# Kernel tuning notes

Measured on AMD Instinct MI355X. Metric: run time of the kernel, lower is better.

## Reference

```python
import jax, jax.numpy as jnp
import numpy as np

B = 8
FEAT = 256
HID = 256
NCLS = 80
SIZES = [(128, 128), (64, 64), (32, 32), (16, 16), (8, 8)]
DELTA_XY = 0.1   # dd_delta_range_xy
DELTA_WH = 2.0   # dd_delta_range_wh
PRIOR_P = 0.01   # prior_cls_prob


def _priors():
    # prior_cxcy: normalized grid centers per pyramid level (sine_pos_encodings id maps,
    # normalize=True with all-ones masks). prior_wh: (1/fW, 1/fH) per level.
    cxcy, wh = [], []
    for (h, w) in SIZES:
        cy = (jnp.arange(h, dtype=jnp.float32) + 0.5) / h
        cx = (jnp.arange(w, dtype=jnp.float32) + 0.5) / w
        gx, gy = jnp.meshgrid(cx, cy, indexing='xy')           # [h, w]
        cxcy.append(jnp.stack([gx, gy], axis=-1).reshape(h * w, 2))
        wh.append(jnp.broadcast_to(jnp.array([1.0 / w, 1.0 / h], jnp.float32), (h * w, 2)))
    return jnp.concatenate(cxcy, axis=0), jnp.concatenate(wh, axis=0)  # [N,2], [N,2]


def _mlp(x, Wh, bh, Wo, bo):
    # Linear(feat->hidden) + ReLU, then Linear(hidden->out)
    h = jax.nn.relu(jnp.einsum('bnf,hf->bnh', x, Wh) + bh)
    return jnp.einsum('bnh,oh->bno', h, Wo) + bo


def setup_inputs() -> dict:
    key = jax.random.key(0)
    ks = jax.random.split(key, 12)
    inp = {}
    for i, (h, w) in enumerate(SIZES):
        inp[f'fm{i}'] = jax.random.normal(ks[i], (B, FEAT, h, w), dtype=jnp.float32)
    s_in = 1.0 / np.sqrt(FEAT)
    s_h = 1.0 / np.sqrt(HID)
    bias_value = float(-np.log((1.0 - PRIOR_P) / PRIOR_P))
    inp['cls_Wh'] = jax.random.normal(ks[5], (HID, FEAT), dtype=jnp.float32) * s_in
    inp['cls_bh'] = jnp.zeros((HID,), jnp.float32)
    inp['cls_Wo'] = jax.random.normal(ks[6], (NCLS, HID), dtype=jnp.float32) * s_h
    inp['cls_bo'] = jnp.full((NCLS,), bias_value, jnp.float32)  # focal prior bias init
    inp['box_Wh'] = jax.random.normal(ks[7], (HID, FEAT), dtype=jnp.float32) * s_in
    inp['box_bh'] = jnp.zeros((HID,), jnp.float32)
    inp['box_Wo'] = jax.random.normal(ks[8], (4, HID), dtype=jnp.float32) * s_h
    inp['box_bo'] = jnp.zeros((4,), jnp.float32)  # zero-init box bias
    return inp


def reference(fm0, fm1, fm2, fm3, fm4,
              cls_Wh, cls_bh, cls_Wo, cls_bo,
              box_Wh, box_bh, box_Wo, box_bo):
    fms = [fm0, fm1, fm2, fm3, fm4]
    # obj_feats: concat of flatten(2).permute(0,2,1) -> [B, N, FEAT]
    obj_feats = jnp.concatenate(
        [f.reshape(B, FEAT, -1).transpose(0, 2, 1) for f in fms], axis=1)
    cls_logits = _mlp(obj_feats, cls_Wh, cls_bh, cls_Wo, cls_bo)   # [B, N, NCLS]
    box_logits = _mlp(obj_feats, box_Wh, box_bh, box_Wo, box_bo)   # [B, N, 4]
    box_deltas = jnp.tanh(box_logits)
    prior_cxcy, prior_wh = _priors()
    pred_cxcy = prior_cxcy[None] + DELTA_XY * box_deltas[:, :, :2]
    pred_wh = prior_wh[None] * (DELTA_WH ** box_deltas[:, :, 2:])
    # pack [cls_logits | pred_boxes(cxcywh)] -> [B, N, NCLS+4]
    return jnp.concatenate([cls_logits, pred_cxcy, pred_wh], axis=-1)
```

## Files before the change

### kernel.cpp

```cpp
#include <hip/hip_runtime.h>
#include <hip/hip_bf16.h>
#include <math.h>
#include <stdint.h>

#define NTOK 21824
#define NTILE128 171

typedef __attribute__((ext_vector_type(8)))  short bf16x8;
typedef __attribute__((ext_vector_type(4)))  float f32x4;
typedef __attribute__((ext_vector_type(16))) float f32x16;

__device__ __forceinline__ uint32_t f2bf(float f) {
    uint32_t u = __builtin_bit_cast(uint32_t, f);
    return (u + 0x7FFFu + ((u >> 16) & 1u)) >> 16;
}
__device__ __forceinline__ uint32_t pkbf2(float lo, float hi) {
    __hip_bfloat162 h = __float22bfloat162_rn(float2{lo, hi});
    uint32_t r; __builtin_memcpy(&r, &h, 4);
    return r;
}

#define WOFF_CWH 0
#define WOFF_BWH 65536
#define WOFF_CWO 131072
#define WOFF_BWO 151552

__global__ void prep_weights(const float* __restrict__ cWh, const float* __restrict__ cWo,
                             const float* __restrict__ bWh, const float* __restrict__ bWo,
                             uint16_t* __restrict__ ws) {
    int i = blockIdx.x * 256 + threadIdx.x;
    if (i >= 155648) return;
    uint32_t v;
    if (i < 65536)       v = f2bf(cWh[i]);
    else if (i < 131072) v = f2bf(bWh[i - 65536]);
    else if (i < 151552) v = f2bf(cWo[i - 131072]);
    else { int j = i - 151552; v = (j < 1024) ? f2bf(bWo[j]) : 0u; }
    ws[i] = (uint16_t)v;
}

__global__ __launch_bounds__(512, 4) void dfd_head(
    const float* __restrict__ fm0, const float* __restrict__ fm1,
    const float* __restrict__ fm2, const float* __restrict__ fm3,
    const float* __restrict__ fm4,
    const float* __restrict__ cls_bh, const float* __restrict__ cls_bo,
    const float* __restrict__ box_bh, const float* __restrict__ box_bo,
    const uint16_t* __restrict__ wbf,
    float* __restrict__ out)
{
    const int g    = blockIdx.x;
    const int s    = g & 15;
    const int tile = (g >> 4) * 8 + (s & 7);
    const int head = s >> 3;
    if (tile >= NTILE128) return;

    __shared__ uint16_t LB[128 * 256];
    uint16_t* Xs = LB;
    uint16_t* Hs = LB;

    const int tid  = threadIdx.x;
    const int lane = tid & 63;
    const int w    = tid >> 6;
    const int r    = lane & 15;
    const int q    = lane >> 4;
    const int col  = lane & 31;
    const int hi   = lane >> 5;
    const int n0   = tile * 128;
    const int b    = blockIdx.y;

    const float* fm; int off, ls;
    if      (n0 < 16384) { fm = fm0; off = 0;     ls = 7; }
    else if (n0 < 20480) { fm = fm1; off = 16384; ls = 6; }
    else if (n0 < 21504) { fm = fm2; off = 20480; ls = 5; }
    else if (n0 < 21760) { fm = fm3; off = 21504; ls = 4; }
    else                 { fm = fm4; off = 21760; ls = 3; }
    const int dim = 1 << ls;
    const int hw  = 1 << (2 * ls);
    const int p0  = n0 - off;
    const int T   = (n0 == 21760) ? 64 : 128;
    const int NT16 = T >> 4;

    {
        const int t  = tid & 127;
        const int fg = tid >> 7;
        const int sw = (t & 31) << 3;
        if (t < T) {
            const float* src = fm + (size_t)b * 256 * hw + p0 + t;
            #pragma unroll
            for (int i = 0; i < 8; ++i) {
                const int f0 = fg * 64 + i * 8;
                float x[8];
                #pragma unroll
                for (int e = 0; e < 8; ++e) x[e] = src[(size_t)(f0 + e) * hw];
                uint4 pk;
                pk.x = pkbf2(x[0], x[1]); pk.y = pkbf2(x[2], x[3]);
                pk.z = pkbf2(x[4], x[5]); pk.w = pkbf2(x[6], x[7]);
                *reinterpret_cast<uint4*>(&Xs[t * 256 + (f0 ^ sw)]) = pk;
            }
        }
    }
    __syncthreads();

    f32x16 acc[4];
    {
        #pragma unroll
        for (int nt = 0; nt < 4; ++nt)
            #pragma unroll
            for (int e = 0; e < 16; ++e) acc[nt][e] = 0.f;

        const int hhw = w * 32;
        const uint16_t* Wbase = wbf + (head ? WOFF_BWH : WOFF_CWH) + hhw * 256;
        const int kh = hi * 8;
        const uint16_t* Wr = Wbase + col * 256 + kh;
        const int sw0 = col << 3;

        #pragma unroll
        for (int ks = 0; ks < 16; ++ks) {
            const bf16x8 a = *(const bf16x8*)(Wr + ks * 16);
            const int kx = (ks * 16 + kh) ^ sw0;
            #pragma unroll
            for (int nt = 0; nt < 4; ++nt) {
                const bf16x8 x = *(const bf16x8*)&Xs[(nt * 32 + col) * 256 + kx];
                acc[nt] = __builtin_amdgcn_mfma_f32_32x32x16_bf16(a, x, acc[nt], 0, 0, 0);
            }
        }
    }
    __syncthreads();

    {
        const int hhw = w * 32;
        const float* bh_ = (head ? box_bh : cls_bh) + hhw;
        #pragma unroll
        for (int nt = 0; nt < 4; ++nt) {
            const int t   = nt * 32 + col;
            const int swt = (t & 15) << 4;
            #pragma unroll
            for (int g2 = 0; g2 < 4; ++g2) {
                const int hb = 8 * g2 + 4 * hi;
                const f32x4 bv = *(const f32x4*)(bh_ + hb);
                const float v0 = fmaxf(acc[nt][4 * g2 + 0] + bv[0], 0.f);
                const float v1 = fmaxf(acc[nt][4 * g2 + 1] + bv[1], 0.f);
                const float v2 = fmaxf(acc[nt][4 * g2 + 2] + bv[2], 0.f);
                const float v3 = fmaxf(acc[nt][4 * g2 + 3] + bv[3], 0.f);
                uint2 pk; pk.x = pkbf2(v0, v1); pk.y = pkbf2(v2, v3);
                *reinterpret_cast<uint2*>(&Hs[t * 256 + ((hhw + hb) ^ swt)]) = pk;
            }
        }
    }
    __syncthreads();

    if (head == 0) {
        if (w < 5) {
            const uint16_t* Bw = wbf + WOFF_CWO + (w * 16 + r) * 256 + q * 8;
            bf16x8 bfr[8];
            #pragma unroll
            for (int kq = 0; kq < 8; ++kq) bfr[kq] = *(const bf16x8*)(Bw + kq * 32);
            const float bo_l = cls_bo[w * 16 + r];
            #pragma unroll
            for (int tt = 0; tt < 8; ++tt) {
                if (tt < NT16) {
                    const int tr  = tt * 16 + r;
                    const int swt = (tr & 15) << 4;
                    const uint16_t* hrow = &Hs[tr * 256];
                    f32x4 c = {0.f, 0.f, 0.f, 0.f};
                    #pragma unroll
                    for (int kq = 0; kq < 8; ++kq) {
                        const bf16x8 a = *(const bf16x8*)&hrow[(kq * 32 + q * 8) ^ swt];
                        c = __builtin_amdgcn_mfma_f32_16x16x32_bf16(a, bfr[kq], c, 0, 0, 0);
                    }
                    #pragma unroll
                    for (int jj = 0; jj < 4; ++jj)
                        out[((size_t)b * NTOK + n0 + tt * 16 + q * 4 + jj) * 84 + w * 16 + r]
                            = c[jj] + bo_l;
                }
            }
        }
    } else {
        if (w < NT16) {
            const uint16_t* Bw = wbf + WOFF_BWO + r * 256 + q * 8;
            const int tr  = w * 16 + r;
            const int swt = (tr & 15) << 4;
            const uint16_t* hrow = &Hs[tr * 256];
            f32x4 c = {0.f, 0.f, 0.f, 0.f};
            #pragma unroll
            for (int kq = 0; kq < 8; ++kq) {
                const bf16x8 a   = *(const bf16x8*)&hrow[(kq * 32 + q * 8) ^ swt];
                const bf16x8 bfr = *(const bf16x8*)(Bw + kq * 32);
                c = __builtin_amdgcn_mfma_f32_16x16x32_bf16(a, bfr, c, 0, 0, 0);
            }
            if (r < 4) {
                const float bo_l = box_bo[r];
                const float inv  = 1.0f / (float)dim;
                #pragma unroll
                for (int jj = 0; jj < 4; ++jj) {
                    const int t2 = w * 16 + q * 4 + jj;
                    const int p  = p0 + t2;
                    const float d = tanhf(c[jj] + bo_l);
                    float val;
                    if (r == 0)      val = ((float)(p & (dim - 1)) + 0.5f) * inv + 0.1f * d;
                    else if (r == 1) val = ((float)(p >> ls) + 0.5f) * inv + 0.1f * d;
                    else             val = exp2f(d) * inv;
                    out[((size_t)b * NTOK + n0 + t2) * 84 + 80 + r] = val;
                }
            }
        }
    }
}

extern "C" void kernel_launch(void* const* d_in, const int* in_sizes, int n_in,
                              void* d_out, int out_size, void* d_ws, size_t ws_size,
                              hipStream_t stream) {
    uint16_t* ws = (uint16_t*)d_ws;
    prep_weights<<<608, 256, 0, stream>>>(
        (const float*)d_in[5],  (const float*)d_in[7],
        (const float*)d_in[9],  (const float*)d_in[11], ws);
    dim3 grid(22 * 16, 8);
    dfd_head<<<grid, 512, 0, stream>>>(
        (const float*)d_in[0], (const float*)d_in[1], (const float*)d_in[2],
        (const float*)d_in[3], (const float*)d_in[4],
        (const float*)d_in[6],  (const float*)d_in[8],
        (const float*)d_in[10], (const float*)d_in[12],
        ws, (float*)d_out);
}
```

Before: 111.0 us.

## Halve token tile and loop over four batches reusing register-resident hidden weights

Token tiles shrink from 128 to 64, and each block now loops over four batch images. The block's slice of the first-layer weight is loaded into registers once and reused across the batches, instead of being reloaded from memory per batch. Separate LDS buffers for the input tile and the hidden activations replace the single aliased buffer. The intent is less weight traffic and more work per block, but the grid drops from 2816 to 1376 blocks and each block runs four batches one after another. Holding 16 extra bf16x8 fragments in registers under launch_bounds(512,4) also risks spills or lower occupancy.

```diff
diff --git a/kernel.cpp b/kernel.cpp
--- a/kernel.cpp
+++ b/kernel.cpp
@@ -4,7 +4,7 @@
 #include <stdint.h>
 
 #define NTOK 21824
-#define NTILE128 171
+#define NTILE 341
 
 typedef __attribute__((ext_vector_type(8)))  short bf16x8;
 typedef __attribute__((ext_vector_type(4)))  float f32x4;
@@ -51,11 +51,10 @@
     const int s    = g & 15;
     const int tile = (g >> 4) * 8 + (s & 7);
     const int head = s >> 3;
-    if (tile >= NTILE128) return;
-
-    __shared__ uint16_t LB[128 * 256];
-    uint16_t* Xs = LB;
-    uint16_t* Hs = LB;
+    if (tile >= NTILE) return;
+
+    __shared__ uint16_t Xs[64 * 256];
+    __shared__ uint16_t Hs[64 * 256];
 
     const int tid  = threadIdx.x;
     const int lane = tid & 63;
@@ -64,8 +63,8 @@
     const int q    = lane >> 4;
     const int col  = lane & 31;
     const int hi   = lane >> 5;
-    const int n0   = tile * 128;
-    const int b    = blockIdx.y;
+    const int n0   = tile * 64;
+    const int b0   = blockIdx.y * 4;
 
     const float* fm; int off, ls;
     if      (n0 < 16384) { fm = fm0; off = 0;     ls = 7; }
@@ -76,18 +75,27 @@
     const int dim = 1 << ls;
     const int hw  = 1 << (2 * ls);
     const int p0  = n0 - off;
-    const int T   = (n0 == 21760) ? 64 : 128;
-    const int NT16 = T >> 4;
-
-    {
-        const int t  = tid & 127;
-        const int fg = tid >> 7;
-        const int sw = (t & 31) << 3;
-        if (t < T) {
+
+    const int hhw = w * 32;
+    const int kh  = hi * 8;
+    const uint16_t* Wr = wbf + (head ? WOFF_BWH : WOFF_CWH) + (hhw + col) * 256 + kh;
+    bf16x8 Wf[16];
+    #pragma unroll
+    for (int ks = 0; ks < 16; ++ks) Wf[ks] = *(const bf16x8*)(Wr + ks * 16);
+
+    const int sw0 = col << 3;
+    const float* bh_ = (head ? box_bh : cls_bh) + hhw;
+
+    for (int lb = 0; lb < 4; ++lb) {
+        const int b = b0 + lb;
+
+        {
+            const int t  = tid & 63;
+            const int sw = (t & 31) << 3;
             const float* src = fm + (size_t)b * 256 * hw + p0 + t;
             #pragma unroll
-            for (int i = 0; i < 8; ++i) {
-                const int f0 = fg * 64 + i * 8;
+            for (int i = 0; i < 4; ++i) {
+                const int f0 = w * 32 + i * 8;
                 float x[8];
                 #pragma unroll
                 for (int e = 0; e < 8; ++e) x[e] = src[(size_t)(f0 + e) * hw];
@@ -97,40 +105,25 @@
                 *reinterpret_cast<uint4*>(&Xs[t * 256 + (f0 ^ sw)]) = pk;
             }
         }
-    }
-    __syncthreads();
-
-    f32x16 acc[4];
-    {
+        __syncthreads();
+
+        f32x16 acc[2];
         #pragma unroll
-        for (int nt = 0; nt < 4; ++nt)
+        for (int nt = 0; nt < 2; ++nt)
             #pragma unroll
             for (int e = 0; e < 16; ++e) acc[nt][e] = 0.f;
 
-        const int hhw = w * 32;
-        const uint16_t* Wbase = wbf + (head ? WOFF_BWH : WOFF_CWH) + hhw * 256;
-        const int kh = hi * 8;
-        const uint16_t* Wr = Wbase + col * 256 + kh;
-        const int sw0 = col << 3;
-
         #pragma unroll
         for (int ks = 0; ks < 16; ++ks) {
-            const bf16x8 a = *(const bf16x8*)(Wr + ks * 16);
             const int kx = (ks * 16 + kh) ^ sw0;
-            #pragma unroll
-            for (int nt = 0; nt < 4; ++nt) {
-                const bf16x8 x = *(const bf16x8*)&Xs[(nt * 32 + col) * 256 + kx];
-                acc[nt] = __builtin_amdgcn_mfma_f32_32x32x16_bf16(a, x, acc[nt], 0, 0, 0);
-            }
-        }
-    }
-    __syncthreads();
-
-    {
-        const int hhw = w * 32;
-        const float* bh_ = (head ? box_bh : cls_bh) + hhw;
+            const bf16x8 x0 = *(const bf16x8*)&Xs[col * 256 + kx];
+            const bf16x8 x1 = *(const bf16x8*)&Xs[(32 + col) * 256 + kx];
+            acc[0] = __builtin_amdgcn_mfma_f32_32x32x16_bf16(Wf[ks], x0, acc[0], 0, 0, 0);
+            acc[1] = __builtin_amdgcn_mfma_f32_32x32x16_bf16(Wf[ks], x1, acc[1], 0, 0, 0);
+        }
+
         #pragma unroll
-        for (int nt = 0; nt < 4; ++nt) {
+        for (int nt = 0; nt < 2; ++nt) {
             const int t   = nt * 32 + col;
             const int swt = (t & 15) << 4;
             #pragma unroll
@@ -145,19 +138,17 @@
                 *reinterpret_cast<uint2*>(&Hs[t * 256 + ((hhw + hb) ^ swt)]) = pk;
             }
         }
-    }
-    __syncthreads();
-
-    if (head == 0) {
-        if (w < 5) {
-            const uint16_t* Bw = wbf + WOFF_CWO + (w * 16 + r) * 256 + q * 8;
-            bf16x8 bfr[8];
-            #pragma unroll
-            for (int kq = 0; kq < 8; ++kq) bfr[kq] = *(const bf16x8*)(Bw + kq * 32);
-            const float bo_l = cls_bo[w * 16 + r];
-            #pragma unroll
-            for (int tt = 0; tt < 8; ++tt) {
-                if (tt < NT16) {
+        __syncthreads();
+
+        if (head == 0) {
+            if (w < 5) {
+                const uint16_t* Bw = wbf + WOFF_CWO + (w * 16 + r) * 256 + q * 8;
+                bf16x8 bfr[8];
+                #pragma unroll
+                for (int kq = 0; kq < 8; ++kq) bfr[kq] = *(const bf16x8*)(Bw + kq * 32);
+                const float bo_l = cls_bo[w * 16 + r];
+                #pragma unroll
+                for (int tt = 0; tt < 4; ++tt) {
                     const int tr  = tt * 16 + r;
                     const int swt = (tr & 15) << 4;
                     const uint16_t* hrow = &Hs[tr * 256];
@@ -173,33 +164,33 @@
                             = c[jj] + bo_l;
                 }
             }
-        }
-    } else {
-        if (w < NT16) {
-            const uint16_t* Bw = wbf + WOFF_BWO + r * 256 + q * 8;
-            const int tr  = w * 16 + r;
-            const int swt = (tr & 15) << 4;
-            const uint16_t* hrow = &Hs[tr * 256];
-            f32x4 c = {0.f, 0.f, 0.f, 0.f};
-            #pragma unroll
-            for (int kq = 0; kq < 8; ++kq) {
-                const bf16x8 a   = *(const bf16x8*)&hrow[(kq * 32 + q * 8) ^ swt];
-                const bf16x8 bfr = *(const bf16x8*)(Bw + kq * 32);
-                c = __builtin_amdgcn_mfma_f32_16x16x32_bf16(a, bfr, c, 0, 0, 0);
-            }
-            if (r < 4) {
-                const float bo_l = box_bo[r];
-                const float inv  = 1.0f / (float)dim;
-                #pragma unroll
-                for (int jj = 0; jj < 4; ++jj) {
-                    const int t2 = w * 16 + q * 4 + jj;
-                    const int p  = p0 + t2;
-                    const float d = tanhf(c[jj] + bo_l);
-                    float val;
-                    if (r == 0)      val = ((float)(p & (dim - 1)) + 0.5f) * inv + 0.1f * d;
-                    else if (r == 1) val = ((float)(p >> ls) + 0.5f) * inv + 0.1f * d;
-                    else             val = exp2f(d) * inv;
-                    out[((size_t)b * NTOK + n0 + t2) * 84 + 80 + r] = val;
+        } else {
+            if (w < 4) {
+                const uint16_t* Bw = wbf + WOFF_BWO + r * 256 + q * 8;
+                const int tr  = w * 16 + r;
+                const int swt = (tr & 15) << 4;
+                const uint16_t* hrow = &Hs[tr * 256];
+                f32x4 c = {0.f, 0.f, 0.f, 0.f};
+                #pragma unroll
+                for (int kq = 0; kq < 8; ++kq) {
+                    const bf16x8 a   = *(const bf16x8*)&hrow[(kq * 32 + q * 8) ^ swt];
+                    const bf16x8 bfr = *(const bf16x8*)(Bw + kq * 32);
+                    c = __builtin_amdgcn_mfma_f32_16x16x32_bf16(a, bfr, c, 0, 0, 0);
+                }
+                if (r < 4) {
+                    const float bo_l = box_bo[r];
+                    const float inv  = 1.0f / (float)dim;
+                    #pragma unroll
+                    for (int jj = 0; jj < 4; ++jj) {
+                        const int t2 = w * 16 + q * 4 + jj;
+                        const int p  = p0 + t2;
+                        const float d = tanhf(c[jj] + bo_l);
+                        float val;
+                        if (r == 0)      val = ((float)(p & (dim - 1)) + 0.5f) * inv + 0.1f * d;
+                        else if (r == 1) val = ((float)(p >> ls) + 0.5f) * inv + 0.1f * d;
+                        else             val = exp2f(d) * inv;
+                        out[((size_t)b * NTOK + n0 + t2) * 84 + 80 + r] = val;
+                    }
                 }
             }
         }
@@ -213,7 +204,7 @@
     prep_weights<<<608, 256, 0, stream>>>(
         (const float*)d_in[5],  (const float*)d_in[7],
         (const float*)d_in[9],  (const float*)d_in[11], ws);
-    dim3 grid(22 * 16, 8);
+    dim3 grid(43 * 16, 2);
     dfd_head<<<grid, 512, 0, stream>>>(
         (const float*)d_in[0], (const float*)d_in[1], (const float*)d_in[2],
         (const float*)d_in[3], (const float*)d_in[4],
```

After: 348.3 us. 3.14x slower.
